# Kernel tuning notes

Measured on AMD Instinct MI355X. Metric: run time of the kernel, lower is better.

Reference implementation:

```python
import jax, jax.numpy as jnp
import numpy as np
import math

NUM_HEADS = 16
HEAD_SIZE = 64
QKT_MEAN = 0.0
QKT_STD = 0.05
APPLY_NOISE = True
NOISE_KEY = jax.random.key(42)


def quantize_activation_8bit(x):
    max_abs = jnp.maximum(jnp.max(jnp.abs(x)), 1e-08)
    scale = max_abs / 127.0
    return jnp.clip(jnp.round(x / scale), -127, 127) * scale


def quantize_weight_4bit(w):
    max_abs = jnp.maximum(jnp.max(jnp.abs(w)), 1e-08)
    scale = max_abs / 7.0
    return jnp.clip(jnp.round(w / scale), -7, 7) * scale


def setup_inputs() -> dict:
    key = jax.random.key(0)
    k1, k2, k3, k4 = jax.random.split(key, 4)
    B, S, D = 4, 1024, 1024
    hidden_states = jax.random.normal(k1, (B, S, D), dtype=jnp.float32)
    attention_mask = jnp.zeros((B, 1, 1, S), dtype=jnp.float32)
    # nn.Linear weights are [out_features, in_features]
    w_scale = 1.0 / math.sqrt(D)
    Wq = jax.random.normal(k2, (D, D), dtype=jnp.float32) * w_scale
    Wk = jax.random.normal(k3, (D, D), dtype=jnp.float32) * w_scale
    Wv = jax.random.normal(k4, (D, D), dtype=jnp.float32) * w_scale
    return {"hidden_states": hidden_states, "attention_mask": attention_mask,
            "Wq": Wq, "Wk": Wk, "Wv": Wv}


def _split_heads(x):
    B, S, _ = x.shape
    return x.reshape(B, S, NUM_HEADS, HEAD_SIZE).transpose(0, 2, 1, 3)  # [B,H,S,Dh]


def reference(hidden_states, attention_mask, Wq, Wk, Wv):
    h_q = quantize_activation_8bit(hidden_states)
    h_k = quantize_activation_8bit(hidden_states)
    Q = _split_heads(jnp.einsum('bsd,od->bso', h_q, quantize_weight_4bit(Wq)))
    K = _split_heads(jnp.einsum('bsd,od->bso', h_k, quantize_weight_4bit(Wk)))
    V = _split_heads(jnp.einsum('bsd,od->bso', hidden_states, quantize_weight_4bit(Wv)))
    qkt = jnp.einsum('bhqd,bhkd->bhqk', Q, K) / math.sqrt(HEAD_SIZE)
    if APPLY_NOISE and QKT_STD > 0:
        noise = jax.random.normal(NOISE_KEY, qkt.shape, dtype=qkt.dtype) * QKT_STD + QKT_MEAN
        qkt = qkt + noise
    qkt = qkt + attention_mask  # [B,1,1,S] broadcasts over [B,H,S,S]
    attn_weights = jax.nn.softmax(qkt, axis=-1)  # dropout is identity in eval
    ctx = jnp.einsum('bhqk,bhkd->bhqd', attn_weights, V)
    B, H, S, Dh = ctx.shape
    ctx = ctx.transpose(0, 2, 1, 3).reshape(B, S, H * Dh)
    return ctx
```

## Files before the change

kernel.cpp:

```cpp
#include <hip/hip_runtime.h>
#include <hip/hip_bf16.h>

typedef unsigned short u16;
typedef unsigned int u32;
typedef __bf16 bf16x8 __attribute__((ext_vector_type(8)));
typedef __bf16 bf16x4 __attribute__((ext_vector_type(4)));
typedef float f32x4 __attribute__((ext_vector_type(4)));

#define MFMA16(a, b, c) __builtin_amdgcn_mfma_f32_16x16x32_bf16((a), (b), (c), 0, 0, 0)

#define GLOAD_LDS16(gp, lp)                                        \
    __builtin_amdgcn_global_load_lds(                              \
        (const __attribute__((address_space(1))) void*)(gp),       \
        (__attribute__((address_space(3))) void*)(lp), 16, 0, 0)

static __device__ __forceinline__ u32 f2bfbits(float f) {
    union { float f; u32 u; } c; c.f = f;
    return (c.u + 0x7FFFu + ((c.u >> 16) & 1u)) >> 16;
}
static __device__ __forceinline__ u32 f2bfbits_exact(float f) {
    union { float f; u32 u; } c; c.f = f;
    return c.u >> 16;
}
static __device__ __forceinline__ u32 pack_bf16x2(float lo, float hi) {
    float2 v; v.x = lo; v.y = hi;
    union { __hip_bfloat162 h; u32 u; } c;
    c.h = __float22bfloat162_rn(v);
    return c.u;
}

static __device__ __forceinline__ u32 rotl_ab(u32 x, int r) {
    return __builtin_amdgcn_alignbit(x, x, 32 - r);
}

static __device__ __forceinline__ float exp2_fast(float x) {
    float r;
    asm("v_exp_f32 %0, %1\n\ts_nop 1" : "=v"(r) : "v"(x));
    return r;
}

static __device__ __forceinline__ void noise_pu8(u32 tk, float* __restrict__ pu) {
    const u32 K1 = 42u, K2 = 0x1BD11BF0u;
    u32 x0[8], x1[8];
#pragma unroll
    for (int d = 0; d < 8; d++) {
        u32 a = tk + (u32)(d < 4 ? d : 12 + d);
        x0[d] = a;
        x1[d] = rotl_ab(a, 13) ^ a;
    }
#define TFR(R)                                             \
    _Pragma("unroll") for (int d = 0; d < 8; d++) {        \
        x0[d] += x1[d];                                    \
        x1[d] = rotl_ab(x1[d], R) ^ x0[d];                 \
    }
#define TFRI(R, A, B)                                      \
    _Pragma("unroll") for (int d = 0; d < 8; d++) {        \
        x1[d] += (B);                                      \
        x0[d] += (A) + x1[d];              \
        x1[d] = rotl_ab(x1[d], R) ^ x0[d];                 \
    }
    TFR(15) TFR(26) TFR(6)
    TFRI(17, K1, K2 + 1u) TFR(29) TFR(16) TFR(24)
    TFRI(13, K2, 2u)      TFR(15) TFR(26) TFR(6)
    TFRI(17, 0u, K1 + 3u) TFR(29) TFR(16) TFR(24)
    TFRI(13, K1, K2 + 4u) TFR(15) TFR(26) TFR(6)
#undef TFR
#undef TFRI
#pragma unroll
    for (int d = 0; d < 8; d++) {
        u32 bits = (x0[d] + K2) ^ (x1[d] + 5u);
        u32 vb = __builtin_amdgcn_alignbit(0x80u, bits, 9);
        float v2 = __uint_as_float(vb);
        float u = v2 - 3.0f;
        float t = fmaf(-u, u, 1.0f);
        float L2 = __log2f(t);
        L2 = fmaxf(L2, -7.2134752f);
        float z = fmaf(L2, -0.69314718f, -2.5f);
        float p = 2.81022636e-08f;
        p = fmaf(p, z, 3.43273939e-07f);
        p = fmaf(p, z, -3.5233877e-06f);
        p = fmaf(p, z, -4.39150654e-06f);
        p = fmaf(p, z, 0.00021858087f);
        p = fmaf(p, z, -0.00125372503f);
        p = fmaf(p, z, -0.00417768164f);
        p = fmaf(p, z, 0.246640727f);
        p = fmaf(p, z, 1.50140941f);
        pu[d] = p * u;
    }
}

__global__ __launch_bounds__(256) void absmax_k(const float* __restrict__ h,
                                                const float* __restrict__ wq,
                                                const float* __restrict__ wk,
                                                const float* __restrict__ wv,
                                                u32* __restrict__ slots) {
    int t = blockIdx.y;
    const float* src = (t == 0) ? h : (t == 1) ? wq : (t == 2) ? wk : wv;
    int n4 = ((t == 0) ? 4096 * 1024 : 1024 * 1024) / 4;
    u32 mx = 0;
    int tid = threadIdx.x;
    for (int i = blockIdx.x * blockDim.x + tid; i < n4; i += gridDim.x * blockDim.x) {
        uint4 v = ((const uint4*)src)[i];
        mx = max(mx, v.x & 0x7FFFFFFFu);
        mx = max(mx, v.y & 0x7FFFFFFFu);
        mx = max(mx, v.z & 0x7FFFFFFFu);
        mx = max(mx, v.w & 0x7FFFFFFFu);
    }
    __shared__ u32 red[256];
    red[tid] = mx;
    __syncthreads();
    for (int s = 128; s > 0; s >>= 1) {
        if (tid < s) red[tid] = max(red[tid], red[tid + s]);
        __syncthreads();
    }
    if (tid == 0) atomicMax(&slots[t], red[0]);
}

__global__ __launch_bounds__(256) void prequant_all(const float* __restrict__ hidden,
                                                    const float* __restrict__ wq,
                                                    const float* __restrict__ wk,
                                                    const float* __restrict__ wv,
                                                    u16* __restrict__ hq,
                                                    u16* __restrict__ hbf,
                                                    u16* __restrict__ wqi,
                                                    u16* __restrict__ wki,
                                                    u16* __restrict__ wvi,
                                                    const u32* __restrict__ slots) {
    int y = blockIdx.y;
    const float* src = (y == 0) ? hidden : (y == 1) ? wq : (y == 2) ? wk : wv;
    u16* dqi = (y == 0) ? hq : (y == 1) ? wqi : (y == 2) ? wki : wvi;
    u16* draw = (y == 0) ? hbf : nullptr;
    float qmax = (y == 0) ? 127.0f : 7.0f;
    int n8 = ((y == 0) ? 4096 * 1024 : 1024 * 1024) / 8;

    float amax = fmaxf(__uint_as_float(slots[y]), 1e-8f);
    float scale = amax / qmax;
    for (int i = blockIdx.x * blockDim.x + threadIdx.x; i < n8; i += gridDim.x * blockDim.x) {
        float4 a = ((const float4*)src)[2 * i];
        float4 b = ((const float4*)src)[2 * i + 1];
        float x[8] = {a.x, a.y, a.z, a.w, b.x, b.y, b.z, b.w};
        u16 qi[8], rw[8];
#pragma unroll
        for (int j = 0; j < 8; j++) {
            float q = fminf(fmaxf(rintf(x[j] / scale), -qmax), qmax);
            qi[j] = (u16)f2bfbits_exact(q);
            rw[j] = (u16)f2bfbits(x[j]);
        }
        *(uint4*)(dqi + 8 * (size_t)i) = *(const uint4*)qi;
        if (draw) *(uint4*)(draw + 8 * (size_t)i) = *(const uint4*)rw;
    }
}

__global__ __launch_bounds__(256, 2) void qkv_gemm_all(const u16* __restrict__ hq,
                                                       const u16* __restrict__ hbf,
                                                       const u16* __restrict__ wqi,
                                                       const u16* __restrict__ wki,
                                                       const u16* __restrict__ wvi,
                                                       const u32* __restrict__ slots,
                                                       u16* __restrict__ Qb,
                                                       u16* __restrict__ Kb,
                                                       u16* __restrict__ Vtb) {
    __shared__ __align__(16) u16 As[128 * 32];
    __shared__ __align__(16) u16 Bs[128 * 32];
    int z = blockIdx.z;
    const u16* A  = (z < 2) ? hq : hbf;
    const u16* Bw = (z == 0) ? wqi : (z == 1) ? wki : wvi;
    u16* outp     = (z == 0) ? Qb : (z == 1) ? Kb : Vtb;
    int transOut = (z == 2);
    float s_a = fmaxf(__uint_as_float(slots[0]), 1e-8f) / 127.0f;
    float s_w = fmaxf(__uint_as_float(slots[z + 1]), 1e-8f) / 7.0f;
    float oscale = (z < 2) ? (s_a * s_w) : s_w;

    int tid = threadIdx.x;
    int mbase = blockIdx.x * 128, nbase = blockIdx.y * 128;
    int lane = tid & 63, w = tid >> 6;
    int wv_m = w & 1, wv_n = w >> 1;
    int quad = lane >> 4, l16 = lane & 15;

    int srow = lane >> 2, scol = (lane & 3) * 8;
    const u16* ag0 = A + (size_t)(mbase + w * 32 + srow) * 1024 + scol;
    const u16* ag1 = A + (size_t)(mbase + w * 32 + 16 + srow) * 1024 + scol;
    const u16* bg0 = Bw + (size_t)(nbase + w * 32 + srow) * 1024 + scol;
    const u16* bg1 = Bw + (size_t)(nbase + w * 32 + 16 + srow) * 1024 + scol;
    u16* al0 = As + w * 1024;
    u16* al1 = As + w * 1024 + 512;
    u16* bl0 = Bs + w * 1024;
    u16* bl1 = Bs + w * 1024 + 512;

    f32x4 acc[4][4];
#pragma unroll
    for (int i = 0; i < 4; i++)
#pragma unroll
        for (int j = 0; j < 4; j++) acc[i][j] = (f32x4){0.f, 0.f, 0.f, 0.f};

    for (int k0 = 0; k0 < 1024; k0 += 32) {
        __syncthreads();
        GLOAD_LDS16(ag0 + k0, al0);
        GLOAD_LDS16(ag1 + k0, al1);
        GLOAD_LDS16(bg0 + k0, bl0);
        GLOAD_LDS16(bg1 + k0, bl1);
        __syncthreads();

        bf16x8 af[4], bfr[4];
#pragma unroll
        for (int mt = 0; mt < 4; mt++)
            af[mt] = *(const bf16x8*)(As + (wv_m * 64 + mt * 16 + l16) * 32 + quad * 8);
#pragma unroll
        for (int nt = 0; nt < 4; nt++)
            bfr[nt] = *(const bf16x8*)(Bs + (wv_n * 64 + nt * 16 + l16) * 32 + quad * 8);
#pragma unroll
        for (int mt = 0; mt < 4; mt++)
#pragma unroll
            for (int nt = 0; nt < 4; nt++)
                acc[mt][nt] = MFMA16(af[mt], bfr[nt], acc[mt][nt]);
    }

#pragma unroll
    for (int mt = 0; mt < 4; mt++)
#pragma unroll
        for (int nt = 0; nt < 4; nt++)
#pragma unroll
            for (int r = 0; r < 4; r++) {
                float val = acc[mt][nt][r] * oscale;
                int m = mbase + wv_m * 64 + mt * 16 + quad * 4 + r;
                int o = nbase + wv_n * 64 + nt * 16 + l16;
                int b = m >> 10, s = m & 1023;
                int hh = o >> 6, dh = o & 63;
                size_t off = transOut ? (((size_t)(b * 16 + hh) * 64 + dh) * 1024 + s)
                                      : (((size_t)(b * 16 + hh) * 1024 + s) * 64 + dh);
                outp[off] = (u16)f2bfbits(val);
            }
}

struct KVTile {
    bf16x8 bk0, bk1, bk2, bk3;
    bf16x4 vlo[4], vhi[4];
};

static __device__ __forceinline__ void load_tile(KVTile& t,
                                                 const u16* __restrict__ Kb,
                                                 const u16* __restrict__ Vb,
                                                 int ks0, int kk, int l16, int quad) {
    const u16* Kt = Kb + (size_t)(ks0 + kk) * 64;
    t.bk0 = *(const bf16x8*)(Kt + l16 * 64 + quad * 8);
    t.bk1 = *(const bf16x8*)(Kt + l16 * 64 + 32 + quad * 8);
    t.bk2 = *(const bf16x8*)(Kt + (16 + l16) * 64 + quad * 8);
    t.bk3 = *(const bf16x8*)(Kt + (16 + l16) * 64 + 32 + quad * 8);
    const u16* Vk = Vb + kk + 4 * quad;
#pragma unroll
    for (int nt = 0; nt < 4; nt++) {
        t.vlo[nt] = *(const bf16x4*)(Vk + (nt * 16 + l16) * 1024);
        t.vhi[nt] = *(const bf16x4*)(Vk + (nt * 16 + l16) * 1024 + 16);
    }
}

static __device__ __forceinline__ void phase(const KVTile& t,
                                             f32x4 (&oacc)[4], f32x4& lacc,
                                             u32 tk, const float* __restrict__ maskb,
                                             int kk, int quad,
                                             bf16x8 aq0, bf16x8 aq1, bf16x8 ones) {
    const float IL2 = 1.4426950408889634f;
    const float C_S = 0.18033688011112042f;
    const float C_N = 0.10201394645f;

    f32x4 mk4 = *(const f32x4*)(maskb + kk + 4 * quad);
    f32x4 mh4 = *(const f32x4*)(maskb + kk + 16 + 4 * quad);
    mk4 = mk4 * IL2;
    mh4 = mh4 * IL2;

    float pu[8];
    noise_pu8(tk, pu);

    f32x4 s0 = (f32x4){0.f, 0.f, 0.f, 0.f};
    f32x4 s1 = (f32x4){0.f, 0.f, 0.f, 0.f};
    s0 = MFMA16(t.bk0, aq0, s0);
    s0 = MFMA16(t.bk1, aq1, s0);
    s1 = MFMA16(t.bk2, aq0, s1);
    s1 = MFMA16(t.bk3, aq1, s1);

    float e[8];
#pragma unroll
    for (int r = 0; r < 4; r++) {
        e[r]     = exp2_fast(fmaf(pu[r],     C_N, fmaf(s0[r], C_S, mk4[r])));
        e[4 + r] = exp2_fast(fmaf(pu[4 + r], C_N, fmaf(s1[r], C_S, mh4[r])));
    }
    union { u32 u[4]; bf16x8 v; } pf;
    pf.u[0] = pack_bf16x2(e[0], e[1]);
    pf.u[1] = pack_bf16x2(e[2], e[3]);
    pf.u[2] = pack_bf16x2(e[4], e[5]);
    pf.u[3] = pack_bf16x2(e[6], e[7]);

#pragma unroll
    for (int nt = 0; nt < 4; nt++) {
        bf16x8 vf = __builtin_shufflevector(t.vlo[nt], t.vhi[nt], 0, 1, 2, 3, 4, 5, 6, 7);
        oacc[nt] = MFMA16(pf.v, vf, oacc[nt]);
    }
    lacc = MFMA16(pf.v, ones, lacc);
}

__global__ __launch_bounds__(256, 4) void attn_kernel(const u16* __restrict__ Q,
                                                      const u16* __restrict__ K,
                                                      const u16* __restrict__ Vt,
                                                      const float* __restrict__ mask,
                                                      float* __restrict__ O0,
                                                      float* __restrict__ O1,
                                                      float* __restrict__ l0,
                                                      float* __restrict__ l1) {
    int qt = blockIdx.x, h = blockIdx.y;
    int b = blockIdx.z & 3, split = blockIdx.z >> 2;
    int bh = b * 16 + h;
    int tid = threadIdx.x, wv = tid >> 6, lane = tid & 63;
    int quad = lane >> 4, l16 = lane & 15;
    int q0 = qt * 64 + wv * 16;
    int ks0 = split * 512;

    const float* maskb = mask + b * 1024 + ks0;

    float* Obuf = split ? O1 : O0;
    float* lbuf = split ? l1 : l0;
    const u16* Qb = Q + (size_t)bh * 1024 * 64;
    const u16* Kb = K + (size_t)bh * 1024 * 64;
    const u16* Vb = Vt + (size_t)bh * 64 * 1024 + ks0;

    bf16x8 aq0 = *(const bf16x8*)(Qb + (q0 + l16) * 64 + quad * 8);
    bf16x8 aq1 = *(const bf16x8*)(Qb + (q0 + l16) * 64 + 32 + quad * 8);

    union { u32 u[4]; bf16x8 v; } ones;
#pragma unroll
    for (int i = 0; i < 4; i++) ones.u[i] = 0x3F803F80u;

    f32x4 oacc[4];
#pragma unroll
    for (int i = 0; i < 4; i++) oacc[i] = (f32x4){0.f, 0.f, 0.f, 0.f};
    f32x4 lacc = (f32x4){0.f, 0.f, 0.f, 0.f};

    u32 tbase = ((u32)(bh * 1024 + q0 + l16)) * 1024u + (u32)ks0 + (u32)(4 * quad) + 42u;

    KVTile t;
    for (int kk = 0; kk < 512; kk += 32) {
        load_tile(t, Kb, Vb, ks0, kk, l16, quad);
        phase(t, oacc, lacc, tbase + (u32)kk, maskb, kk, quad, aq0, aq1, ones.v);
    }

    if (l16 == 0) {
        int lbase = bh * 1024 + q0 + quad * 4;
#pragma unroll
        for (int r = 0; r < 4; r++) lbuf[lbase + r] = lacc[r];
    }
#pragma unroll
    for (int nt = 0; nt < 4; nt++) {
#pragma unroll
        for (int r = 0; r < 4; r++) {
            int q = q0 + quad * 4 + r;
            int dh = nt * 16 + l16;
            Obuf[((size_t)(b * 1024 + q)) * 1024 + h * 64 + dh] = oacc[nt][r];
        }
    }
}

__global__ __launch_bounds__(256) void combine_k(float* __restrict__ outp,
                                                 const float* __restrict__ O1,
                                                 const float* __restrict__ l0,
                                                 const float* __restrict__ l1) {
    int gid = blockIdx.x * 256 + threadIdx.x;
    int e = gid << 2;
    int bq = e >> 10;
    int h = (e & 1023) >> 6;
    int b = bq >> 10, q = bq & 1023;
    int lidx = ((b * 16 + h) << 10) + q;
    float linv = 1.0f / (l0[lidx] + l1[lidx]);
    float4 a = ((const float4*)outp)[gid];
    float4 c = ((const float4*)O1)[gid];
    float4 o;
    o.x = (a.x + c.x) * linv;
    o.y = (a.y + c.y) * linv;
    o.z = (a.z + c.z) * linv;
    o.w = (a.w + c.w) * linv;
    ((float4*)outp)[gid] = o;
}

extern "C" void kernel_launch(void* const* d_in, const int* in_sizes, int n_in,
                              void* d_out, int out_size, void* d_ws, size_t ws_size,
                              hipStream_t stream) {
    (void)in_sizes; (void)n_in; (void)out_size; (void)ws_size;
    const float* hidden = (const float*)d_in[0];
    const float* maskp  = (const float*)d_in[1];
    const float* Wq     = (const float*)d_in[2];
    const float* Wk     = (const float*)d_in[3];
    const float* Wv     = (const float*)d_in[4];
    float* outp = (float*)d_out;

    char* ws = (char*)d_ws;
    u32* slots = (u32*)ws;
    u16* hq  = (u16*)(ws + 256);
    u16* hbf = hq + 4096 * 1024;
    u16* wqi = hbf + 4096 * 1024;
    u16* wki = wqi + 1024 * 1024;
    u16* wvi = wki + 1024 * 1024;
    u16* Qb  = wvi + 1024 * 1024;
    u16* Kb  = Qb + 4096 * 1024;
    u16* Vtb = Kb + 4096 * 1024;

    float* O1buf = (float*)hq;
    float* l0buf = (float*)wqi;
    float* l1buf = l0buf + 4 * 16 * 1024;

    hipMemsetAsync(slots, 0, 16, stream);
    absmax_k<<<dim3(128, 4), 256, 0, stream>>>(hidden, Wq, Wk, Wv, slots);
    prequant_all<<<dim3(64, 4), 256, 0, stream>>>(hidden, Wq, Wk, Wv,
                                                  hq, hbf, wqi, wki, wvi, slots);
    qkv_gemm_all<<<dim3(32, 8, 3), 256, 0, stream>>>(hq, hbf, wqi, wki, wvi, slots,
                                                     Qb, Kb, Vtb);
    attn_kernel<<<dim3(16, 16, 8), 256, 0, stream>>>(Qb, Kb, Vtb, maskp,
                                                     outp, O1buf, l0buf, l1buf);
    combine_k<<<dim3(4096), 256, 0, stream>>>(outp, O1buf, l0buf, l1buf);
}
```

Baseline: 355.4 us.

## Stage K/V tiles through double-buffered LDS with async global-to-LDS loads

Replaces the per-wave direct global loads of K and V tiles with cooperative global_load_lds copies into a double-buffered shared-memory tile. All four waves in the block share each K/V tile, and the next tile is prefetched while the current one is computed. The scaled mask is also precomputed once into LDS. This removes redundant per-wave global traffic and overlaps load latency with compute, at the cost of a block-wide barrier per iteration and extra LDS use, which may limit occupancy.

```diff
diff --git a/kernel.cpp b/kernel.cpp
--- a/kernel.cpp
+++ b/kernel.cpp
@@ -232,72 +232,6 @@
             }
 }
 
-struct KVTile {
-    bf16x8 bk0, bk1, bk2, bk3;
-    bf16x4 vlo[4], vhi[4];
-};
-
-static __device__ __forceinline__ void load_tile(KVTile& t,
-                                                 const u16* __restrict__ Kb,
-                                                 const u16* __restrict__ Vb,
-                                                 int ks0, int kk, int l16, int quad) {
-    const u16* Kt = Kb + (size_t)(ks0 + kk) * 64;
-    t.bk0 = *(const bf16x8*)(Kt + l16 * 64 + quad * 8);
-    t.bk1 = *(const bf16x8*)(Kt + l16 * 64 + 32 + quad * 8);
-    t.bk2 = *(const bf16x8*)(Kt + (16 + l16) * 64 + quad * 8);
-    t.bk3 = *(const bf16x8*)(Kt + (16 + l16) * 64 + 32 + quad * 8);
-    const u16* Vk = Vb + kk + 4 * quad;
-#pragma unroll
-    for (int nt = 0; nt < 4; nt++) {
-        t.vlo[nt] = *(const bf16x4*)(Vk + (nt * 16 + l16) * 1024);
-        t.vhi[nt] = *(const bf16x4*)(Vk + (nt * 16 + l16) * 1024 + 16);
-    }
-}
-
-static __device__ __forceinline__ void phase(const KVTile& t,
-                                             f32x4 (&oacc)[4], f32x4& lacc,
-                                             u32 tk, const float* __restrict__ maskb,
-                                             int kk, int quad,
-                                             bf16x8 aq0, bf16x8 aq1, bf16x8 ones) {
-    const float IL2 = 1.4426950408889634f;
-    const float C_S = 0.18033688011112042f;
-    const float C_N = 0.10201394645f;
-
-    f32x4 mk4 = *(const f32x4*)(maskb + kk + 4 * quad);
-    f32x4 mh4 = *(const f32x4*)(maskb + kk + 16 + 4 * quad);
-    mk4 = mk4 * IL2;
-    mh4 = mh4 * IL2;
-
-    float pu[8];
-    noise_pu8(tk, pu);
-
-    f32x4 s0 = (f32x4){0.f, 0.f, 0.f, 0.f};
-    f32x4 s1 = (f32x4){0.f, 0.f, 0.f, 0.f};
-    s0 = MFMA16(t.bk0, aq0, s0);
-    s0 = MFMA16(t.bk1, aq1, s0);
-    s1 = MFMA16(t.bk2, aq0, s1);
-    s1 = MFMA16(t.bk3, aq1, s1);
-
-    float e[8];
-#pragma unroll
-    for (int r = 0; r < 4; r++) {
-        e[r]     = exp2_fast(fmaf(pu[r],     C_N, fmaf(s0[r], C_S, mk4[r])));
-        e[4 + r] = exp2_fast(fmaf(pu[4 + r], C_N, fmaf(s1[r], C_S, mh4[r])));
-    }
-    union { u32 u[4]; bf16x8 v; } pf;
-    pf.u[0] = pack_bf16x2(e[0], e[1]);
-    pf.u[1] = pack_bf16x2(e[2], e[3]);
-    pf.u[2] = pack_bf16x2(e[4], e[5]);
-    pf.u[3] = pack_bf16x2(e[6], e[7]);
-
-#pragma unroll
-    for (int nt = 0; nt < 4; nt++) {
-        bf16x8 vf = __builtin_shufflevector(t.vlo[nt], t.vhi[nt], 0, 1, 2, 3, 4, 5, 6, 7);
-        oacc[nt] = MFMA16(pf.v, vf, oacc[nt]);
-    }
-    lacc = MFMA16(pf.v, ones, lacc);
-}
-
 __global__ __launch_bounds__(256, 4) void attn_kernel(const u16* __restrict__ Q,
                                                       const u16* __restrict__ K,
                                                       const u16* __restrict__ Vt,
@@ -306,6 +240,10 @@
                                                       float* __restrict__ O1,
                                                       float* __restrict__ l0,
                                                       float* __restrict__ l1) {
+    __shared__ __align__(16) u16 Ks[2][32 * 64];
+    __shared__ __align__(16) u16 Vs[2][64 * 32];
+    __shared__ __align__(16) float msk2[512];
+
     int qt = blockIdx.x, h = blockIdx.y;
     int b = blockIdx.z & 3, split = blockIdx.z >> 2;
     int bh = b * 16 + h;
@@ -314,7 +252,13 @@
     int q0 = qt * 64 + wv * 16;
     int ks0 = split * 512;
 
+    const float IL2 = 1.4426950408889634f;
+    const float C_S = 0.18033688011112042f;
+    const float C_N = 0.10201394645f;
+
     const float* maskb = mask + b * 1024 + ks0;
+    msk2[tid] = maskb[tid] * IL2;
+    msk2[tid + 256] = maskb[tid + 256] * IL2;
 
     float* Obuf = split ? O1 : O0;
     float* lbuf = split ? l1 : l0;
@@ -336,10 +280,66 @@
 
     u32 tbase = ((u32)(bh * 1024 + q0 + l16)) * 1024u + (u32)ks0 + (u32)(4 * quad) + 42u;
 
-    KVTile t;
+    const u16* kgsrc = Kb + (size_t)(ks0 + wv * 8 + (lane >> 3)) * 64 + (lane & 7) * 8;
+    const u16* vgsrc = Vb + (size_t)(wv * 16 + (lane >> 2)) * 1024 + (lane & 3) * 8;
+    u16* kdst0 = &Ks[0][wv * 512];
+    u16* kdst1 = &Ks[1][wv * 512];
+    u16* vdst0 = &Vs[0][wv * 512];
+    u16* vdst1 = &Vs[1][wv * 512];
+
+    GLOAD_LDS16(kgsrc, kdst0);
+    GLOAD_LDS16(vgsrc, vdst0);
+    __syncthreads();
+
     for (int kk = 0; kk < 512; kk += 32) {
-        load_tile(t, Kb, Vb, ks0, kk, l16, quad);
-        phase(t, oacc, lacc, tbase + (u32)kk, maskb, kk, quad, aq0, aq1, ones.v);
+        int cur = (kk >> 5) & 1;
+        if (kk + 32 < 512) {
+            GLOAD_LDS16(kgsrc + (kk + 32) * 64, cur ? kdst0 : kdst1);
+            GLOAD_LDS16(vgsrc + (kk + 32),     cur ? vdst0 : vdst1);
+        }
+        const u16* Kc = cur ? Ks[1] : Ks[0];
+        const u16* Vc = cur ? Vs[1] : Vs[0];
+
+        f32x4 mk4 = *(const f32x4*)(msk2 + kk + 4 * quad);
+        f32x4 mh4 = *(const f32x4*)(msk2 + kk + 16 + 4 * quad);
+
+        float pu[8];
+        noise_pu8(tbase + (u32)kk, pu);
+
+        bf16x8 bk0 = *(const bf16x8*)(Kc + l16 * 64 + quad * 8);
+        bf16x8 bk1 = *(const bf16x8*)(Kc + l16 * 64 + 32 + quad * 8);
+        bf16x8 bk2 = *(const bf16x8*)(Kc + (16 + l16) * 64 + quad * 8);
+        bf16x8 bk3 = *(const bf16x8*)(Kc + (16 + l16) * 64 + 32 + quad * 8);
+
+        f32x4 s0 = (f32x4){0.f, 0.f, 0.f, 0.f};
+        f32x4 s1 = (f32x4){0.f, 0.f, 0.f, 0.f};
+        s0 = MFMA16(bk0, aq0, s0);
+        s0 = MFMA16(bk1, aq1, s0);
+        s1 = MFMA16(bk2, aq0, s1);
+        s1 = MFMA16(bk3, aq1, s1);
+
+        float e[8];
+#pragma unroll
+        for (int r = 0; r < 4; r++) {
+            e[r]     = exp2_fast(fmaf(pu[r],     C_N, fmaf(s0[r], C_S, mk4[r])));
+            e[4 + r] = exp2_fast(fmaf(pu[4 + r], C_N, fmaf(s1[r], C_S, mh4[r])));
+        }
+        union { u32 u[4]; bf16x8 v; } pf;
+        pf.u[0] = pack_bf16x2(e[0], e[1]);
+        pf.u[1] = pack_bf16x2(e[2], e[3]);
+        pf.u[2] = pack_bf16x2(e[4], e[5]);
+        pf.u[3] = pack_bf16x2(e[6], e[7]);
+
+#pragma unroll
+        for (int nt = 0; nt < 4; nt++) {
+            bf16x4 vlo = *(const bf16x4*)(Vc + (nt * 16 + l16) * 32 + quad * 4);
+            bf16x4 vhi = *(const bf16x4*)(Vc + (nt * 16 + l16) * 32 + 16 + quad * 4);
+            bf16x8 vf = __builtin_shufflevector(vlo, vhi, 0, 1, 2, 3, 4, 5, 6, 7);
+            oacc[nt] = MFMA16(pf.v, vf, oacc[nt]);
+        }
+        lacc = MFMA16(pf.v, ones.v, lacc);
+
+        __syncthreads();
     }
 
     if (l16 == 0) {
```

Measured after the change: 345.3 us. 1.03x faster.
